# Kernel optimization log

Hardware: AMD Instinct MI355X
Metric: run time of the kernel (lower is better)

The kernel has to match this reference:

```python
import jax, jax.numpy as jnp
import numpy as np

V, BLOCK, L, H, E, B, T = 1024, 2048, 4, 8, 512, 4, 2048
D = E // H  # head dim = 64

def setup_inputs() -> dict:
    key = jax.random.key(0)
    ks = jax.random.split(key, 8)
    s = 0.02
    return {
        "idx": jax.random.randint(ks[0], (B, T), 0, V),
        "wte": jax.random.normal(ks[1], (V, E), jnp.float32) * s,
        "wpe": jax.random.normal(ks[2], (BLOCK, E), jnp.float32) * s,
        "ln1_w": jnp.ones((L, E), jnp.float32),
        "ln1_b": jnp.zeros((L, E), jnp.float32),
        "attn_w": jax.random.normal(ks[3], (L, 3 * E, E), jnp.float32) * s,
        "attn_b": jnp.zeros((L, 3 * E), jnp.float32),
        "proj_w": jax.random.normal(ks[4], (L, E, E), jnp.float32) * s,
        "proj_b": jnp.zeros((L, E), jnp.float32),
        "ln2_w": jnp.ones((L, E), jnp.float32),
        "ln2_b": jnp.zeros((L, E), jnp.float32),
        "fc_w": jax.random.normal(ks[5], (L, 4 * E, E), jnp.float32) * s,
        "fc_b": jnp.zeros((L, 4 * E), jnp.float32),
        "fc2_w": jax.random.normal(ks[6], (L, E, 4 * E), jnp.float32) * s,
        "fc2_b": jnp.zeros((L, E), jnp.float32),
        "lnf_w": jnp.ones((E,), jnp.float32),
        "lnf_b": jnp.zeros((E,), jnp.float32),
    }

def layer_norm(x, w, b, eps=1e-5):
    mu = jnp.mean(x, axis=-1, keepdims=True)
    var = jnp.var(x, axis=-1, keepdims=True)
    return (x - mu) * jax.lax.rsqrt(var + eps) * w + b

def reference(idx, wte, wpe, ln1_w, ln1_b, attn_w, attn_b, proj_w, proj_b,
              ln2_w, ln2_b, fc_w, fc_b, fc2_w, fc2_b, lnf_w, lnf_b):
    b, t = idx.shape
    x = wte[idx] + wpe[:t]  # (B,T,E)
    causal = jnp.tril(jnp.ones((t, t), bool))
    scale = 1.0 / np.sqrt(D)

    def block(x, p):
        l1w, l1b, aw, ab, pw, pb, l2w, l2b, fw, fb, f2w, f2b = p
        h = layer_norm(x, l1w, l1b)
        qkv = h @ aw.T + ab  # (B,T,3E)
        q, k, v = jnp.split(qkv, 3, axis=-1)
        q = q.reshape(b, t, H, D)
        k = k.reshape(b, t, H, D)
        v = v.reshape(b, t, H, D)
        att = jnp.einsum('bqhd,bkhd->bhqk', q, k) * scale
        att = jnp.where(causal, att, -jnp.inf)
        att = jax.nn.softmax(att, axis=-1)
        y = jnp.einsum('bhqk,bkhd->bqhd', att, v).reshape(b, t, E)
        x = x + y @ pw.T + pb
        h2 = layer_norm(x, l2w, l2b)
        h2 = jax.nn.gelu(h2 @ fw.T + fb, approximate=False)
        x = x + h2 @ f2w.T + f2b
        return x, None

    params = (ln1_w, ln1_b, attn_w, attn_b, proj_w, proj_b,
              ln2_w, ln2_b, fc_w, fc_b, fc2_w, fc2_b)
    x, _ = jax.lax.scan(block, x, params)
    x = layer_norm(x, lnf_w, lnf_b)
    logits = x @ wte.T  # tied lm_head
    return logits
```

## Files before the change

kernel.cpp:

```cpp
#include <hip/hip_runtime.h>
#include <hip/hip_bf16.h>
#include <math.h>

#define B_ 4
#define T_ 2048
#define E_ 512
#define H_ 8
#define D_ 64
#define L_ 4
#define V_ 1024
#define NROWS (B_*T_)
#define KBLK 64
#define KVPAD 72
#define PPAD 72

typedef __hip_bfloat16 bf16;
typedef __attribute__((ext_vector_type(8))) short bf16x8;
typedef __attribute__((ext_vector_type(4))) float f32x4;

__device__ __forceinline__ short f2bf_s(float f) {
    union { bf16 h; short s; } t; t.h = __float2bfloat16(f); return t.s;
}

__device__ __forceinline__ void gload_lds16(const bf16* g, bf16* l) {
    __builtin_amdgcn_global_load_lds((const __attribute__((address_space(1))) void*)g,
                                     (__attribute__((address_space(3))) void*)l, 16, 0, 0);
}

__device__ __forceinline__ float gelu_fast(float v) {
    float u = v * (0.7978845608028654f * (1.0f + 0.044715f * v * v));
    float t = 1.0f - 2.0f / (__expf(2.0f * u) + 1.0f);
    return 0.5f * v * (1.0f + t);
}

__global__ void f2bf_all(const float* __restrict__ s0, const float* __restrict__ s1,
                         const float* __restrict__ s2, const float* __restrict__ s3,
                         const float* __restrict__ s4, bf16* __restrict__ dst) {
    size_t gi = (size_t)blockIdx.x * 1024 + threadIdx.x * 4;
    const float* src; size_t off;
    if (blockIdx.x < 3072)       { src = s0; off = gi; }
    else if (blockIdx.x < 4096)  { src = s1; off = gi - (size_t)3072 * 1024; }
    else if (blockIdx.x < 8192)  { src = s2; off = gi - (size_t)4096 * 1024; }
    else if (blockIdx.x < 12288) { src = s3; off = gi - (size_t)8192 * 1024; }
    else                         { src = s4; off = gi - (size_t)12288 * 1024; }
    float4 v = *(const float4*)(src + off);
    union { bf16 h[4]; uint2 u; } t;
    t.h[0] = __float2bfloat16(v.x); t.h[1] = __float2bfloat16(v.y);
    t.h[2] = __float2bfloat16(v.z); t.h[3] = __float2bfloat16(v.w);
    *(uint2*)(dst + gi) = t.u;
}

__global__ void embed_kernel(const int* __restrict__ idx, const float* __restrict__ wte,
                             const float* __restrict__ wpe, float* __restrict__ x) {
    int i = (blockIdx.x * blockDim.x + threadIdx.x) * 4;
    int row = i >> 9;
    int e = i & (E_ - 1);
    int t = row & (T_ - 1);
    int id = idx[row];
    float4 a = *(const float4*)(wte + (size_t)id * E_ + e);
    float4 p = *(const float4*)(wpe + (size_t)t * E_ + e);
    a.x += p.x; a.y += p.y; a.z += p.z; a.w += p.w;
    *(float4*)(x + i) = a;
}

__global__ __launch_bounds__(512) void layernorm_kernel(const float* __restrict__ x,
                                 const float* __restrict__ w, const float* __restrict__ b,
                                 bf16* __restrict__ out) {
    int wid = threadIdx.x >> 6, lane = threadIdx.x & 63;
    int row = blockIdx.x * 8 + wid;
    const float* xr = x + (size_t)row * E_ + lane * 8;
    float4 a0 = *(const float4*)xr;
    float4 a1 = *(const float4*)(xr + 4);
    float s = (a0.x + a0.y) + (a0.z + a0.w) + (a1.x + a1.y) + (a1.z + a1.w);
    float q = a0.x*a0.x + a0.y*a0.y + a0.z*a0.z + a0.w*a0.w
            + a1.x*a1.x + a1.y*a1.y + a1.z*a1.z + a1.w*a1.w;
    #pragma unroll
    for (int st = 1; st < 64; st <<= 1) { s += __shfl_xor(s, st); q += __shfl_xor(q, st); }
    float mean = s * (1.0f / E_);
    float var = q * (1.0f / E_) - mean * mean;
    float rstd = rsqrtf(var + 1e-5f);
    float4 w0 = *(const float4*)(w + lane * 8), w1 = *(const float4*)(w + lane * 8 + 4);
    float4 b0 = *(const float4*)(b + lane * 8), b1 = *(const float4*)(b + lane * 8 + 4);
    union { bf16 h[8]; uint4 u; } o;
    o.h[0] = __float2bfloat16((a0.x - mean) * rstd * w0.x + b0.x);
    o.h[1] = __float2bfloat16((a0.y - mean) * rstd * w0.y + b0.y);
    o.h[2] = __float2bfloat16((a0.z - mean) * rstd * w0.z + b0.z);
    o.h[3] = __float2bfloat16((a0.w - mean) * rstd * w0.w + b0.w);
    o.h[4] = __float2bfloat16((a1.x - mean) * rstd * w1.x + b1.x);
    o.h[5] = __float2bfloat16((a1.y - mean) * rstd * w1.y + b1.y);
    o.h[6] = __float2bfloat16((a1.z - mean) * rstd * w1.z + b1.z);
    o.h[7] = __float2bfloat16((a1.w - mean) * rstd * w1.w + b1.w);
    *(uint4*)(out + (size_t)row * E_ + lane * 8) = o.u;
}

template<int ACT, int OMODE, bool BIAS, bool QKV>
__global__ __launch_bounds__(256) void gemm_mfma(const bf16* __restrict__ A, const bf16* __restrict__ W,
        const float* __restrict__ bias, float* __restrict__ Cf, bf16* __restrict__ Cb,
        bf16* __restrict__ Vt, int M, int N, int K) {
    __shared__ __align__(16) bf16 As[2][128][32];
    __shared__ __align__(16) bf16 Bs[2][128][32];
    int tid = threadIdx.x;
    int lane = tid & 63, wid = tid >> 6;
    int wm = (wid >> 1) * 64, wn = (wid & 1) * 64;
    int m0 = blockIdx.y * 128, n0 = blockIdx.x * 128;

    int srow = wid * 32 + (lane >> 2);
    int scol = (lane & 3) * 8;
    const bf16* ga = A + (size_t)(m0 + srow) * K + scol;
    const bf16* gb = W + (size_t)(n0 + srow) * K + scol;
    int fr = lane & 15, fk = (lane >> 4) * 8;

    f32x4 acc[4][4];
    #pragma unroll
    for (int i = 0; i < 4; ++i)
        #pragma unroll
        for (int j = 0; j < 4; ++j) acc[i][j] = (f32x4){0.f, 0.f, 0.f, 0.f};

    gload_lds16(ga,          &As[0][wid * 32][0]);
    gload_lds16(ga + 16 * K, &As[0][wid * 32 + 16][0]);
    gload_lds16(gb,          &Bs[0][wid * 32][0]);
    gload_lds16(gb + 16 * K, &Bs[0][wid * 32 + 16][0]);
    __syncthreads();

    const int nst = K >> 5;
    for (int t = 0; t < nst; ++t) {
        const int cur = t & 1;
        if (t + 1 < nst) {
            const bf16* ga2 = ga + (t + 1) * 32;
            const bf16* gb2 = gb + (t + 1) * 32;
            gload_lds16(ga2,          &As[cur ^ 1][wid * 32][0]);
            gload_lds16(ga2 + 16 * K, &As[cur ^ 1][wid * 32 + 16][0]);
            gload_lds16(gb2,          &Bs[cur ^ 1][wid * 32][0]);
            gload_lds16(gb2 + 16 * K, &Bs[cur ^ 1][wid * 32 + 16][0]);
        }
        bf16x8 af[4], bff[4];
        #pragma unroll
        for (int i = 0; i < 4; ++i) af[i]  = *(const bf16x8*)&As[cur][wm + i * 16 + fr][fk];
        #pragma unroll
        for (int j = 0; j < 4; ++j) bff[j] = *(const bf16x8*)&Bs[cur][wn + j * 16 + fr][fk];
        #pragma unroll
        for (int i = 0; i < 4; ++i)
            #pragma unroll
            for (int j = 0; j < 4; ++j)
                acc[i][j] = __builtin_amdgcn_mfma_f32_16x16x32_bf16(af[i], bff[j], acc[i][j], 0, 0, 0);
        __syncthreads();
    }

    int orow = m0 + wm + (lane >> 4) * 4;
    int ocol = n0 + wn + (lane & 15);

    if (QKV && n0 >= 2 * E_) {
        #pragma unroll
        for (int i = 0; i < 4; ++i) {
            int rowb = orow + i * 16;
            int bb = rowb >> 11;
            int t0 = rowb & (T_ - 1);
            #pragma unroll
            for (int j = 0; j < 4; ++j) {
                int col = ocol + j * 16;
                int dg = col - 2 * E_;
                int hh = dg >> 6, dd = dg & 63;
                float bv = BIAS ? bias[col] : 0.0f;
                union { bf16 h[4]; short4 s4; } pk;
                #pragma unroll
                for (int r = 0; r < 4; ++r)
                    pk.h[r] = __float2bfloat16(acc[i][j][r] + bv);
                *(short4*)&Vt[(((size_t)bb * H_ + hh) * D_ + dd) * T_ + t0] = pk.s4;
            }
        }
        return;
    }

    #pragma unroll
    for (int i = 0; i < 4; ++i) {
        #pragma unroll
        for (int j = 0; j < 4; ++j) {
            #pragma unroll
            for (int r = 0; r < 4; ++r) {
                int row = orow + i * 16 + r;
                int col = ocol + j * 16;
                float v = acc[i][j][r];
                if (BIAS) v += bias[col];
                if (ACT == 1) v = gelu_fast(v);
                if (QKV) {
                    if (col < E_) v *= 0.125f;
                    Cb[(size_t)row * (2 * E_) + col] = __float2bfloat16(v);
                } else {
                    size_t off = (size_t)row * N + col;
                    if (OMODE == 0) Cf[off] = v;
                    else if (OMODE == 1) Cb[off] = __float2bfloat16(v);
                    else Cf[off] += v;
                }
            }
        }
    }
}

template<int OMODE, bool BIAS>
__global__ __launch_bounds__(256) void gemm_mfma64(const bf16* __restrict__ A, const bf16* __restrict__ W,
        const float* __restrict__ bias, float* __restrict__ Cf, bf16* __restrict__ Cb,
        int M, int N, int K) {
    __shared__ __align__(16) bf16 As[2][64][32];
    __shared__ __align__(16) bf16 Bs[2][64][32];
    int tid = threadIdx.x;
    int lane = tid & 63, wid = tid >> 6;
    int wm = (wid >> 1) * 32, wn = (wid & 1) * 32;
    int m0 = blockIdx.y * 64, n0 = blockIdx.x * 64;

    int srow = wid * 16 + (lane >> 2);
    int scol = (lane & 3) * 8;
    const bf16* ga = A + (size_t)(m0 + srow) * K + scol;
    const bf16* gb = W + (size_t)(n0 + srow) * K + scol;
    int fr = lane & 15, fk = (lane >> 4) * 8;

    f32x4 acc[2][2];
    #pragma unroll
    for (int i = 0; i < 2; ++i)
        #pragma unroll
        for (int j = 0; j < 2; ++j) acc[i][j] = (f32x4){0.f, 0.f, 0.f, 0.f};

    gload_lds16(ga, &As[0][wid * 16][0]);
    gload_lds16(gb, &Bs[0][wid * 16][0]);
    __syncthreads();

    const int nst = K >> 5;
    for (int t = 0; t < nst; ++t) {
        const int cur = t & 1;
        if (t + 1 < nst) {
            gload_lds16(ga + (t + 1) * 32, &As[cur ^ 1][wid * 16][0]);
            gload_lds16(gb + (t + 1) * 32, &Bs[cur ^ 1][wid * 16][0]);
        }
        bf16x8 af[2], bff[2];
        #pragma unroll
        for (int i = 0; i < 2; ++i) af[i]  = *(const bf16x8*)&As[cur][wm + i * 16 + fr][fk];
        #pragma unroll
        for (int j = 0; j < 2; ++j) bff[j] = *(const bf16x8*)&Bs[cur][wn + j * 16 + fr][fk];
        #pragma unroll
        for (int i = 0; i < 2; ++i)
            #pragma unroll
            for (int j = 0; j < 2; ++j)
                acc[i][j] = __builtin_amdgcn_mfma_f32_16x16x32_bf16(af[i], bff[j], acc[i][j], 0, 0, 0);
        __syncthreads();
    }

    int orow = m0 + wm + (lane >> 4) * 4;
    int ocol = n0 + wn + (lane & 15);
    #pragma unroll
    for (int i = 0; i < 2; ++i) {
        #pragma unroll
        for (int j = 0; j < 2; ++j) {
            #pragma unroll
            for (int r = 0; r < 4; ++r) {
                int row = orow + i * 16 + r;
                int col = ocol + j * 16;
                float v = acc[i][j][r];
                if (BIAS) v += bias[col];
                size_t off = (size_t)row * N + col;
                if (OMODE == 0) Cf[off] = v;
                else if (OMODE == 1) Cb[off] = __float2bfloat16(v);
                else Cf[off] += v;
            }
        }
    }
}

template<bool DOMASK>
__device__ __forceinline__ void attn_tile(
        const short (&Ks)[KBLK][KVPAD], const short (&VsT)[D_][KVPAD],
        short (*Psw)[PPAD], const bf16x8 (&qf)[2],
        float& m_run, float& l_run, f32x4 (&accO)[4],
        int fr, int fg, int k0, int qrow) {
    f32x4 st[4];
    __builtin_amdgcn_s_setprio(1);
    #pragma unroll
    for (int j = 0; j < 4; ++j) {
        f32x4 a = (f32x4){0.f, 0.f, 0.f, 0.f};
        #pragma unroll
        for (int kk = 0; kk < 2; ++kk) {
            bf16x8 kf = *(const bf16x8*)&Ks[j * 16 + fr][kk * 32 + fg * 8];
            a = __builtin_amdgcn_mfma_f32_16x16x32_bf16(kf, qf[kk], a, 0, 0, 0);
        }
        st[j] = a;
    }
    __builtin_amdgcn_s_setprio(0);
    float mx = -INFINITY;
    #pragma unroll
    for (int j = 0; j < 4; ++j)
        #pragma unroll
        for (int r = 0; r < 4; ++r) {
            if (DOMASK && (k0 + j * 16 + fg * 4 + r > qrow)) st[j][r] = -INFINITY;
            mx = fmaxf(mx, st[j][r]);
        }
    mx = fmaxf(mx, __shfl_xor(mx, 16));
    mx = fmaxf(mx, __shfl_xor(mx, 32));
    if (!__all(mx <= m_run + 8.0f)) {
        float mnew = fmaxf(m_run, mx);
        float corr = __expf(m_run - mnew);
        l_run *= corr;
        #pragma unroll
        for (int r = 0; r < 4; ++r) {
            float cr = __shfl(corr, fg * 4 + r);
            #pragma unroll
            for (int n = 0; n < 4; ++n) accO[n][r] *= cr;
        }
        m_run = mnew;
    }
    float rl = 0.0f;
    #pragma unroll
    for (int j = 0; j < 4; ++j) {
        float p0 = __expf(st[j][0] - m_run), p1 = __expf(st[j][1] - m_run);
        float p2 = __expf(st[j][2] - m_run), p3 = __expf(st[j][3] - m_run);
        rl += (p0 + p1) + (p2 + p3);
        short4 pk;
        pk.x = f2bf_s(p0); pk.y = f2bf_s(p1); pk.z = f2bf_s(p2); pk.w = f2bf_s(p3);
        *(short4*)&Psw[fr][j * 16 + fg * 4] = pk;
    }
    rl += __shfl_xor(rl, 16);
    rl += __shfl_xor(rl, 32);
    l_run += rl;
    __builtin_amdgcn_s_setprio(1);
    bf16x8 pa[2];
    #pragma unroll
    for (int kk = 0; kk < 2; ++kk)
        pa[kk] = *(const bf16x8*)&Psw[fr][kk * 32 + fg * 8];
    #pragma unroll
    for (int n = 0; n < 4; ++n)
        #pragma unroll
        for (int kk = 0; kk < 2; ++kk) {
            bf16x8 vb = *(const bf16x8*)&VsT[n * 16 + fr][kk * 32 + fg * 8];
            accO[n] = __builtin_amdgcn_mfma_f32_16x16x32_bf16(pa[kk], vb, accO[n], 0, 0, 0);
        }
    __builtin_amdgcn_s_setprio(0);
}

__global__ __launch_bounds__(256, 4) void attn_mfma(const bf16* __restrict__ qk,
                                                    const bf16* __restrict__ vt,
                                                    bf16* __restrict__ y) {
    __shared__ __align__(16) short Ks[KBLK][KVPAD];
    __shared__ __align__(16) short VsT[D_][KVPAD];
    __shared__ __align__(16) short Ps[4][16][PPAD];
    const int qi = (gridDim.x - 1) - blockIdx.x;
    const int h = blockIdx.y, b = blockIdx.z;
    const int q0 = qi * 64;
    const int tid = threadIdx.x;
    const int lane = tid & 63, wid = tid >> 6;
    const int fr = lane & 15, fg = lane >> 4;
    const int qmin = q0 + wid * 16;
    const int qrow = qmin + fr;

    const int sr0 = tid >> 3;
    const int sc = (tid & 7) * 8;
    const bf16* kst = qk + (size_t)(b * T_ + sr0) * (2 * E_) + E_ + h * D_ + sc;
    const bf16* vst = vt + ((size_t)(b * H_ + h) * D_ + sr0) * T_ + sc;

    const bf16* qbase = qk + (size_t)(b * T_ + qrow) * (2 * E_) + h * D_;
    bf16x8 qf[2];
    #pragma unroll
    for (int kk = 0; kk < 2; ++kk)
        qf[kk] = *(const bf16x8*)(qbase + kk * 32 + fg * 8);

    float m_run = -INFINITY, l_run = 0.0f;
    f32x4 accO[4];
    #pragma unroll
    for (int n = 0; n < 4; ++n) accO[n] = (f32x4){0.f, 0.f, 0.f, 0.f};

    const int ntiles = qi + 1;

    {
        uint4 k0r = *(const uint4*)kst;
        uint4 k1r = *(const uint4*)(kst + 32 * (2 * E_));
        uint4 v0r = *(const uint4*)vst;
        uint4 v1r = *(const uint4*)(vst + 32 * T_);
        *(uint4*)&Ks[sr0][sc] = k0r;  *(uint4*)&Ks[sr0 + 32][sc] = k1r;
        *(uint4*)&VsT[sr0][sc] = v0r; *(uint4*)&VsT[sr0 + 32][sc] = v1r;
    }
    __syncthreads();

    for (int kt = 0; kt < ntiles; ++kt) {
        const bool have_next = (kt + 1 < ntiles);
        uint4 nk0, nk1, nv0, nv1;
        if (have_next) {
            const bf16* kn = kst + (size_t)(kt + 1) * KBLK * (2 * E_);
            const bf16* vn = vst + (kt + 1) * KBLK;
            nk0 = *(const uint4*)kn; nk1 = *(const uint4*)(kn + 32 * (2 * E_));
            nv0 = *(const uint4*)vn; nv1 = *(const uint4*)(vn + 32 * T_);
        }

        if (kt + 1 == ntiles)
            attn_tile<true >(Ks, VsT, Ps[wid], qf, m_run, l_run, accO, fr, fg, kt * KBLK, qrow);
        else
            attn_tile<false>(Ks, VsT, Ps[wid], qf, m_run, l_run, accO, fr, fg, kt * KBLK, qrow);

        __syncthreads();
        if (have_next) {
            *(uint4*)&Ks[sr0][sc] = nk0;  *(uint4*)&Ks[sr0 + 32][sc] = nk1;
            *(uint4*)&VsT[sr0][sc] = nv0; *(uint4*)&VsT[sr0 + 32][sc] = nv1;
            __syncthreads();
        }
    }

    float linv = 1.0f / l_run;
    #pragma unroll
    for (int r = 0; r < 4; ++r) {
        float lr = __shfl(linv, fg * 4 + r);
        int gq = qmin + fg * 4 + r;
        #pragma unroll
        for (int n = 0; n < 4; ++n)
            y[(size_t)(b * T_ + gq) * E_ + h * D_ + n * 16 + fr] =
                __float2bfloat16(accO[n][r] * lr);
    }
}

extern "C" void kernel_launch(void* const* d_in, const int* in_sizes, int n_in,
                              void* d_out, int out_size, void* d_ws, size_t ws_size,
                              hipStream_t stream) {
    const int*   idx    = (const int*)d_in[0];
    const float* wte    = (const float*)d_in[1];
    const float* wpe    = (const float*)d_in[2];
    const float* ln1_w  = (const float*)d_in[3];
    const float* ln1_b  = (const float*)d_in[4];
    const float* attn_w = (const float*)d_in[5];
    const float* attn_b = (const float*)d_in[6];
    const float* proj_w = (const float*)d_in[7];
    const float* proj_b = (const float*)d_in[8];
    const float* ln2_w  = (const float*)d_in[9];
    const float* ln2_b  = (const float*)d_in[10];
    const float* fc_w   = (const float*)d_in[11];
    const float* fc_b   = (const float*)d_in[12];
    const float* fc2_w  = (const float*)d_in[13];
    const float* fc2_b  = (const float*)d_in[14];
    const float* lnf_w  = (const float*)d_in[15];
    const float* lnf_b  = (const float*)d_in[16];
    float* out = (float*)d_out;

    float* x   = (float*)d_ws;
    bf16* hbf  = (bf16*)(x + (size_t)NROWS * E_);
    bf16* big  = hbf + (size_t)NROWS * E_;
    bf16* qkb  = big;
    bf16* vtb  = big + (size_t)NROWS * 2 * E_;
    bf16* wb   = big + (size_t)NROWS * 4 * E_;
    bf16* attn_wb = wb;
    bf16* proj_wb = attn_wb + (size_t)L_ * 3 * E_ * E_;
    bf16* fc_wb   = proj_wb + (size_t)L_ * E_ * E_;
    bf16* fc2_wb  = fc_wb   + (size_t)L_ * 4 * E_ * E_;
    bf16* wte_b   = fc2_wb  + (size_t)L_ * E_ * 4 * E_;

    f2bf_all<<<12800, 256, 0, stream>>>(attn_w, proj_w, fc_w, fc2_w, wte, wb);
    embed_kernel<<<NROWS * E_ / 1024, 256, 0, stream>>>(idx, wte, wpe, x);

    for (int l = 0; l < L_; ++l) {
        layernorm_kernel<<<NROWS / 8, 512, 0, stream>>>(x, ln1_w + l * E_, ln1_b + l * E_, hbf);
        gemm_mfma<0, 1, true, true><<<dim3(3 * E_ / 128, NROWS / 128), 256, 0, stream>>>(
            hbf, attn_wb + (size_t)l * 3 * E_ * E_, attn_b + l * 3 * E_, nullptr, qkb, vtb,
            NROWS, 3 * E_, E_);
        attn_mfma<<<dim3(T_ / 64, H_, B_), 256, 0, stream>>>(qkb, vtb, hbf);
        gemm_mfma64<2, true><<<dim3(E_ / 64, NROWS / 64), 256, 0, stream>>>(
            hbf, proj_wb + (size_t)l * E_ * E_, proj_b + l * E_, x, nullptr,
            NROWS, E_, E_);
        layernorm_kernel<<<NROWS / 8, 512, 0, stream>>>(x, ln2_w + l * E_, ln2_b + l * E_, hbf);
        gemm_mfma<1, 1, true, false><<<dim3(4 * E_ / 128, NROWS / 128), 256, 0, stream>>>(
            hbf, fc_wb + (size_t)l * 4 * E_ * E_, fc_b + l * 4 * E_, nullptr, big, nullptr,
            NROWS, 4 * E_, E_);
        gemm_mfma64<2, true><<<dim3(E_ / 64, NROWS / 64), 256, 0, stream>>>(
            big, fc2_wb + (size_t)l * E_ * 4 * E_, fc2_b + l * E_, x, nullptr,
            NROWS, E_, 4 * E_);
    }
    layernorm_kernel<<<NROWS / 8, 512, 0, stream>>>(x, lnf_w, lnf_b, hbf);
    gemm_mfma64<0, false><<<dim3(V_ / 64, NROWS / 64), 256, 0, stream>>>(
        hbf, wte_b, nullptr, out, nullptr, NROWS, V_, E_);
}
```

Before: 869.0 us.

## Use persistent atomic work queue for attention and 64-tile QKV GEMM

Attention becomes a persistent kernel of 1280 blocks that pull (q-tile, head, batch) items from a global atomic counter, largest causal tiles first, to balance the triangular workload across CUs. The occupancy hint rises from 4 to 5 blocks per CU. The QKV projection moves from the 128x128 GEMM to the 64x64 GEMM, which now handles the QKV scaling and V-transpose epilogue, giving more blocks for better CU fill. In exchange it adds a memset and atomic traffic, and the smaller tile gives less operand reuse for QKV.

```diff
diff --git a/kernel.cpp b/kernel.cpp
--- a/kernel.cpp
+++ b/kernel.cpp
@@ -13,6 +13,8 @@
 #define KBLK 64
 #define KVPAD 72
 #define PPAD 72
+#define NPERS 1280
+#define NITEMS 1024
 
 typedef __hip_bfloat16 bf16;
 typedef __attribute__((ext_vector_type(8))) short bf16x8;
@@ -93,10 +95,10 @@
     *(uint4*)(out + (size_t)row * E_ + lane * 8) = o.u;
 }
 
-template<int ACT, int OMODE, bool BIAS, bool QKV>
+template<int ACT, int OMODE, bool BIAS>
 __global__ __launch_bounds__(256) void gemm_mfma(const bf16* __restrict__ A, const bf16* __restrict__ W,
         const float* __restrict__ bias, float* __restrict__ Cf, bf16* __restrict__ Cb,
-        bf16* __restrict__ Vt, int M, int N, int K) {
+        int M, int N, int K) {
     __shared__ __align__(16) bf16 As[2][128][32];
     __shared__ __align__(16) bf16 Bs[2][128][32];
     int tid = threadIdx.x;
@@ -148,15 +150,84 @@
 
     int orow = m0 + wm + (lane >> 4) * 4;
     int ocol = n0 + wn + (lane & 15);
+    #pragma unroll
+    for (int i = 0; i < 4; ++i) {
+        #pragma unroll
+        for (int j = 0; j < 4; ++j) {
+            #pragma unroll
+            for (int r = 0; r < 4; ++r) {
+                int row = orow + i * 16 + r;
+                int col = ocol + j * 16;
+                float v = acc[i][j][r];
+                if (BIAS) v += bias[col];
+                if (ACT == 1) v = gelu_fast(v);
+                size_t off = (size_t)row * N + col;
+                if (OMODE == 0) Cf[off] = v;
+                else if (OMODE == 1) Cb[off] = __float2bfloat16(v);
+                else Cf[off] += v;
+            }
+        }
+    }
+}
+
+template<int ACT, int OMODE, bool BIAS, bool QKV>
+__global__ __launch_bounds__(256) void gemm_mfma64(const bf16* __restrict__ A, const bf16* __restrict__ W,
+        const float* __restrict__ bias, float* __restrict__ Cf, bf16* __restrict__ Cb,
+        bf16* __restrict__ Vt, int M, int N, int K) {
+    __shared__ __align__(16) bf16 As[2][64][32];
+    __shared__ __align__(16) bf16 Bs[2][64][32];
+    int tid = threadIdx.x;
+    int lane = tid & 63, wid = tid >> 6;
+    int wm = (wid >> 1) * 32, wn = (wid & 1) * 32;
+    int m0 = blockIdx.y * 64, n0 = blockIdx.x * 64;
+
+    int srow = wid * 16 + (lane >> 2);
+    int scol = (lane & 3) * 8;
+    const bf16* ga = A + (size_t)(m0 + srow) * K + scol;
+    const bf16* gb = W + (size_t)(n0 + srow) * K + scol;
+    int fr = lane & 15, fk = (lane >> 4) * 8;
+
+    f32x4 acc[2][2];
+    #pragma unroll
+    for (int i = 0; i < 2; ++i)
+        #pragma unroll
+        for (int j = 0; j < 2; ++j) acc[i][j] = (f32x4){0.f, 0.f, 0.f, 0.f};
+
+    gload_lds16(ga, &As[0][wid * 16][0]);
+    gload_lds16(gb, &Bs[0][wid * 16][0]);
+    __syncthreads();
+
+    const int nst = K >> 5;
+    for (int t = 0; t < nst; ++t) {
+        const int cur = t & 1;
+        if (t + 1 < nst) {
+            gload_lds16(ga + (t + 1) * 32, &As[cur ^ 1][wid * 16][0]);
+            gload_lds16(gb + (t + 1) * 32, &Bs[cur ^ 1][wid * 16][0]);
+        }
+        bf16x8 af[2], bff[2];
+        #pragma unroll
+        for (int i = 0; i < 2; ++i) af[i]  = *(const bf16x8*)&As[cur][wm + i * 16 + fr][fk];
+        #pragma unroll
+        for (int j = 0; j < 2; ++j) bff[j] = *(const bf16x8*)&Bs[cur][wn + j * 16 + fr][fk];
+        #pragma unroll
+        for (int i = 0; i < 2; ++i)
+            #pragma unroll
+            for (int j = 0; j < 2; ++j)
+                acc[i][j] = __builtin_amdgcn_mfma_f32_16x16x32_bf16(af[i], bff[j], acc[i][j], 0, 0, 0);
+        __syncthreads();
+    }
+
+    int orow = m0 + wm + (lane >> 4) * 4;
+    int ocol = n0 + wn + (lane & 15);
 
     if (QKV && n0 >= 2 * E_) {
         #pragma unroll
-        for (int i = 0; i < 4; ++i) {
+        for (int i = 0; i < 2; ++i) {
             int rowb = orow + i * 16;
             int bb = rowb >> 11;
             int t0 = rowb & (T_ - 1);
             #pragma unroll
-            for (int j = 0; j < 4; ++j) {
+            for (int j = 0; j < 2; ++j) {
                 int col = ocol + j * 16;
                 int dg = col - 2 * E_;
                 int hh = dg >> 6, dd = dg & 63;
@@ -172,9 +243,9 @@
     }
 
     #pragma unroll
-    for (int i = 0; i < 4; ++i) {
-        #pragma unroll
-        for (int j = 0; j < 4; ++j) {
+    for (int i = 0; i < 2; ++i) {
+        #pragma unroll
+        for (int j = 0; j < 2; ++j) {
             #pragma unroll
             for (int r = 0; r < 4; ++r) {
                 int row = orow + i * 16 + r;
@@ -196,74 +267,6 @@
     }
 }
 
-template<int OMODE, bool BIAS>
-__global__ __launch_bounds__(256) void gemm_mfma64(const bf16* __restrict__ A, const bf16* __restrict__ W,
-        const float* __restrict__ bias, float* __restrict__ Cf, bf16* __restrict__ Cb,
-        int M, int N, int K) {
-    __shared__ __align__(16) bf16 As[2][64][32];
-    __shared__ __align__(16) bf16 Bs[2][64][32];
-    int tid = threadIdx.x;
-    int lane = tid & 63, wid = tid >> 6;
-    int wm = (wid >> 1) * 32, wn = (wid & 1) * 32;
-    int m0 = blockIdx.y * 64, n0 = blockIdx.x * 64;
-
-    int srow = wid * 16 + (lane >> 2);
-    int scol = (lane & 3) * 8;
-    const bf16* ga = A + (size_t)(m0 + srow) * K + scol;
-    const bf16* gb = W + (size_t)(n0 + srow) * K + scol;
-    int fr = lane & 15, fk = (lane >> 4) * 8;
-
-    f32x4 acc[2][2];
-    #pragma unroll
-    for (int i = 0; i < 2; ++i)
-        #pragma unroll
-        for (int j = 0; j < 2; ++j) acc[i][j] = (f32x4){0.f, 0.f, 0.f, 0.f};
-
-    gload_lds16(ga, &As[0][wid * 16][0]);
-    gload_lds16(gb, &Bs[0][wid * 16][0]);
-    __syncthreads();
-
-    const int nst = K >> 5;
-    for (int t = 0; t < nst; ++t) {
-        const int cur = t & 1;
-        if (t + 1 < nst) {
-            gload_lds16(ga + (t + 1) * 32, &As[cur ^ 1][wid * 16][0]);
-            gload_lds16(gb + (t + 1) * 32, &Bs[cur ^ 1][wid * 16][0]);
-        }
-        bf16x8 af[2], bff[2];
-        #pragma unroll
-        for (int i = 0; i < 2; ++i) af[i]  = *(const bf16x8*)&As[cur][wm + i * 16 + fr][fk];
-        #pragma unroll
-        for (int j = 0; j < 2; ++j) bff[j] = *(const bf16x8*)&Bs[cur][wn + j * 16 + fr][fk];
-        #pragma unroll
-        for (int i = 0; i < 2; ++i)
-            #pragma unroll
-            for (int j = 0; j < 2; ++j)
-                acc[i][j] = __builtin_amdgcn_mfma_f32_16x16x32_bf16(af[i], bff[j], acc[i][j], 0, 0, 0);
-        __syncthreads();
-    }
-
-    int orow = m0 + wm + (lane >> 4) * 4;
-    int ocol = n0 + wn + (lane & 15);
-    #pragma unroll
-    for (int i = 0; i < 2; ++i) {
-        #pragma unroll
-        for (int j = 0; j < 2; ++j) {
-            #pragma unroll
-            for (int r = 0; r < 4; ++r) {
-                int row = orow + i * 16 + r;
-                int col = ocol + j * 16;
-                float v = acc[i][j][r];
-                if (BIAS) v += bias[col];
-                size_t off = (size_t)row * N + col;
-                if (OMODE == 0) Cf[off] = v;
-                else if (OMODE == 1) Cb[off] = __float2bfloat16(v);
-                else Cf[off] += v;
-            }
-        }
-    }
-}
-
 template<bool DOMASK>
 __device__ __forceinline__ void attn_tile(
         const short (&Ks)[KBLK][KVPAD], const short (&VsT)[D_][KVPAD],
@@ -333,81 +336,89 @@
     __builtin_amdgcn_s_setprio(0);
 }
 
-__global__ __launch_bounds__(256, 4) void attn_mfma(const bf16* __restrict__ qk,
+__global__ __launch_bounds__(256, 5) void attn_mfma(const bf16* __restrict__ qk,
                                                     const bf16* __restrict__ vt,
-                                                    bf16* __restrict__ y) {
+                                                    bf16* __restrict__ y,
+                                                    int* __restrict__ counter) {
     __shared__ __align__(16) short Ks[KBLK][KVPAD];
     __shared__ __align__(16) short VsT[D_][KVPAD];
     __shared__ __align__(16) short Ps[4][16][PPAD];
-    const int qi = (gridDim.x - 1) - blockIdx.x;
-    const int h = blockIdx.y, b = blockIdx.z;
-    const int q0 = qi * 64;
+    __shared__ int item_s;
     const int tid = threadIdx.x;
     const int lane = tid & 63, wid = tid >> 6;
     const int fr = lane & 15, fg = lane >> 4;
-    const int qmin = q0 + wid * 16;
-    const int qrow = qmin + fr;
-
     const int sr0 = tid >> 3;
     const int sc = (tid & 7) * 8;
-    const bf16* kst = qk + (size_t)(b * T_ + sr0) * (2 * E_) + E_ + h * D_ + sc;
-    const bf16* vst = vt + ((size_t)(b * H_ + h) * D_ + sr0) * T_ + sc;
-
-    const bf16* qbase = qk + (size_t)(b * T_ + qrow) * (2 * E_) + h * D_;
-    bf16x8 qf[2];
-    #pragma unroll
-    for (int kk = 0; kk < 2; ++kk)
-        qf[kk] = *(const bf16x8*)(qbase + kk * 32 + fg * 8);
-
-    float m_run = -INFINITY, l_run = 0.0f;
-    f32x4 accO[4];
-    #pragma unroll
-    for (int n = 0; n < 4; ++n) accO[n] = (f32x4){0.f, 0.f, 0.f, 0.f};
-
-    const int ntiles = qi + 1;
-
-    {
-        uint4 k0r = *(const uint4*)kst;
-        uint4 k1r = *(const uint4*)(kst + 32 * (2 * E_));
-        uint4 v0r = *(const uint4*)vst;
-        uint4 v1r = *(const uint4*)(vst + 32 * T_);
-        *(uint4*)&Ks[sr0][sc] = k0r;  *(uint4*)&Ks[sr0 + 32][sc] = k1r;
-        *(uint4*)&VsT[sr0][sc] = v0r; *(uint4*)&VsT[sr0 + 32][sc] = v1r;
-    }
-    __syncthreads();
-
-    for (int kt = 0; kt < ntiles; ++kt) {
-        const bool have_next = (kt + 1 < ntiles);
-        uint4 nk0, nk1, nv0, nv1;
-        if (have_next) {
-            const bf16* kn = kst + (size_t)(kt + 1) * KBLK * (2 * E_);
-            const bf16* vn = vst + (kt + 1) * KBLK;
-            nk0 = *(const uint4*)kn; nk1 = *(const uint4*)(kn + 32 * (2 * E_));
-            nv0 = *(const uint4*)vn; nv1 = *(const uint4*)(vn + 32 * T_);
-        }
-
-        if (kt + 1 == ntiles)
-            attn_tile<true >(Ks, VsT, Ps[wid], qf, m_run, l_run, accO, fr, fg, kt * KBLK, qrow);
-        else
-            attn_tile<false>(Ks, VsT, Ps[wid], qf, m_run, l_run, accO, fr, fg, kt * KBLK, qrow);
-
+
+    for (;;) {
+        if (tid == 0) item_s = atomicAdd(counter, 1);
         __syncthreads();
-        if (have_next) {
-            *(uint4*)&Ks[sr0][sc] = nk0;  *(uint4*)&Ks[sr0 + 32][sc] = nk1;
-            *(uint4*)&VsT[sr0][sc] = nv0; *(uint4*)&VsT[sr0 + 32][sc] = nv1;
+        const int it = item_s;
+        if (it >= NITEMS) break;
+        const int qi = 31 - (it >> 5);
+        const int h = (it & 31) >> 2, b = it & 3;
+        const int q0 = qi * 64;
+        const int qmin = q0 + wid * 16;
+        const int qrow = qmin + fr;
+
+        const bf16* kst = qk + (size_t)(b * T_ + sr0) * (2 * E_) + E_ + h * D_ + sc;
+        const bf16* vst = vt + ((size_t)(b * H_ + h) * D_ + sr0) * T_ + sc;
+        const bf16* qbase = qk + (size_t)(b * T_ + qrow) * (2 * E_) + h * D_;
+        bf16x8 qf[2];
+        #pragma unroll
+        for (int kk = 0; kk < 2; ++kk)
+            qf[kk] = *(const bf16x8*)(qbase + kk * 32 + fg * 8);
+
+        float m_run = -INFINITY, l_run = 0.0f;
+        f32x4 accO[4];
+        #pragma unroll
+        for (int n = 0; n < 4; ++n) accO[n] = (f32x4){0.f, 0.f, 0.f, 0.f};
+
+        const int ntiles = qi + 1;
+
+        {
+            uint4 k0r = *(const uint4*)kst;
+            uint4 k1r = *(const uint4*)(kst + 32 * (2 * E_));
+            uint4 v0r = *(const uint4*)vst;
+            uint4 v1r = *(const uint4*)(vst + 32 * T_);
+            *(uint4*)&Ks[sr0][sc] = k0r;  *(uint4*)&Ks[sr0 + 32][sc] = k1r;
+            *(uint4*)&VsT[sr0][sc] = v0r; *(uint4*)&VsT[sr0 + 32][sc] = v1r;
+        }
+        __syncthreads();
+
+        for (int kt = 0; kt < ntiles; ++kt) {
+            const bool have_next = (kt + 1 < ntiles);
+            uint4 nk0, nk1, nv0, nv1;
+            if (have_next) {
+                const bf16* kn = kst + (size_t)(kt + 1) * KBLK * (2 * E_);
+                const bf16* vn = vst + (kt + 1) * KBLK;
+                nk0 = *(const uint4*)kn; nk1 = *(const uint4*)(kn + 32 * (2 * E_));
+                nv0 = *(const uint4*)vn; nv1 = *(const uint4*)(vn + 32 * T_);
+            }
+
+            if (kt + 1 == ntiles)
+                attn_tile<true >(Ks, VsT, Ps[wid], qf, m_run, l_run, accO, fr, fg, kt * KBLK, qrow);
+            else
+                attn_tile<false>(Ks, VsT, Ps[wid], qf, m_run, l_run, accO, fr, fg, kt * KBLK, qrow);
+
             __syncthreads();
-        }
-    }
-
-    float linv = 1.0f / l_run;
-    #pragma unroll
-    for (int r = 0; r < 4; ++r) {
-        float lr = __shfl(linv, fg * 4 + r);
-        int gq = qmin + fg * 4 + r;
-        #pragma unroll
-        for (int n = 0; n < 4; ++n)
-            y[(size_t)(b * T_ + gq) * E_ + h * D_ + n * 16 + fr] =
-                __float2bfloat16(accO[n][r] * lr);
+            if (have_next) {
+                *(uint4*)&Ks[sr0][sc] = nk0;  *(uint4*)&Ks[sr0 + 32][sc] = nk1;
+                *(uint4*)&VsT[sr0][sc] = nv0; *(uint4*)&VsT[sr0 + 32][sc] = nv1;
+                __syncthreads();
+            }
+        }
+
+        float linv = 1.0f / l_run;
+        #pragma unroll
+        for (int r = 0; r < 4; ++r) {
+            float lr = __shfl(linv, fg * 4 + r);
+            int gq = qmin + fg * 4 + r;
+            #pragma unroll
+            for (int n = 0; n < 4; ++n)
+                y[(size_t)(b * T_ + gq) * E_ + h * D_ + n * 16 + fr] =
+                    __float2bfloat16(accO[n][r] * lr);
+        }
     }
 }
 
@@ -444,28 +455,30 @@
     bf16* fc_wb   = proj_wb + (size_t)L_ * E_ * E_;
     bf16* fc2_wb  = fc_wb   + (size_t)L_ * 4 * E_ * E_;
     bf16* wte_b   = fc2_wb  + (size_t)L_ * E_ * 4 * E_;
-
+    int*  counters = (int*)(wte_b + (size_t)V_ * E_);
+
+    hipMemsetAsync(counters, 0, 4 * sizeof(int), stream);
     f2bf_all<<<12800, 256, 0, stream>>>(attn_w, proj_w, fc_w, fc2_w, wte, wb);
     embed_kernel<<<NROWS * E_ / 1024, 256, 0, stream>>>(idx, wte, wpe, x);
 
     for (int l = 0; l < L_; ++l) {
         layernorm_kernel<<<NROWS / 8, 512, 0, stream>>>(x, ln1_w + l * E_, ln1_b + l * E_, hbf);
-        gemm_mfma<0, 1, true, true><<<dim3(3 * E_ / 128, NROWS / 128), 256, 0, stream>>>(
+        gemm_mfma64<0, 1, true, true><<<dim3(3 * E_ / 64, NROWS / 64), 256, 0, stream>>>(
             hbf, attn_wb + (size_t)l * 3 * E_ * E_, attn_b + l * 3 * E_, nullptr, qkb, vtb,
             NROWS, 3 * E_, E_);
-        attn_mfma<<<dim3(T_ / 64, H_, B_), 256, 0, stream>>>(qkb, vtb, hbf);
-        gemm_mfma64<2, true><<<dim3(E_ / 64, NROWS / 64), 256, 0, stream>>>(
-            hbf, proj_wb + (size_t)l * E_ * E_, proj_b + l * E_, x, nullptr,
+        attn_mfma<<<NPERS, 256, 0, stream>>>(qkb, vtb, hbf, counters + l);
+        gemm_mfma64<0, 2, true, false><<<dim3(E_ / 64, NROWS / 64), 256, 0, stream>>>(
+            hbf, proj_wb + (size_t)l * E_ * E_, proj_b + l * E_, x, nullptr, nullptr,
             NROWS, E_, E_);
         layernorm_kernel<<<NROWS / 8, 512, 0, stream>>>(x, ln2_w + l * E_, ln2_b + l * E_, hbf);
-        gemm_mfma<1, 1, true, false><<<dim3(4 * E_ / 128, NROWS / 128), 256, 0, stream>>>(
-            hbf, fc_wb + (size_t)l * 4 * E_ * E_, fc_b + l * 4 * E_, nullptr, big, nullptr,
+        gemm_mfma<1, 1, true><<<dim3(4 * E_ / 128, NROWS / 128), 256, 0, stream>>>(
+            hbf, fc_wb + (size_t)l * 4 * E_ * E_, fc_b + l * 4 * E_, nullptr, big,
             NROWS, 4 * E_, E_);
-        gemm_mfma64<2, true><<<dim3(E_ / 64, NROWS / 64), 256, 0, stream>>>(
-            big, fc2_wb + (size_t)l * E_ * 4 * E_, fc2_b + l * E_, x, nullptr,
+        gemm_mfma64<0, 2, true, false><<<dim3(E_ / 64, NROWS / 64), 256, 0, stream>>>(
+            big, fc2_wb + (size_t)l * E_ * 4 * E_, fc2_b + l * E_, x, nullptr, nullptr,
             NROWS, E_, 4 * E_);
     }
     layernorm_kernel<<<NROWS / 8, 512, 0, stream>>>(x, lnf_w, lnf_b, hbf);
-    gemm_mfma64<0, false><<<dim3(V_ / 64, NROWS / 64), 256, 0, stream>>>(
-        hbf, wte_b, nullptr, out, nullptr, NROWS, V_, E_);
-}
+    gemm_mfma64<0, 0, false, false><<<dim3(V_ / 64, NROWS / 64), 256, 0, stream>>>(
+        hbf, wte_b, nullptr, out, nullptr, nullptr, NROWS, V_, E_);
+}
```

New measurement: 906.8 us. +4.3%, slower.
